# Optimization experiments

Measured on AMD Instinct MI355X. Metric: run time of the kernel, lower is better.

Reference implementation:

```python
import jax, jax.numpy as jnp
import numpy as np

H = 64  # hidden size
I = 1   # input size


def setup_inputs() -> dict:
    key = jax.random.key(0)
    ks = jax.random.split(key, 7)
    B, T = 4096, 512
    s_ih = 1.0 / np.sqrt(H)
    x = jax.random.normal(ks[0], (B, T, I), dtype=jnp.float32)
    # torch nn.GRU params: weight_ih [3H, I], weight_hh [3H, H], biases [3H]
    W_ih = jax.random.uniform(ks[1], (3 * H, I), minval=-s_ih, maxval=s_ih, dtype=jnp.float32)
    W_hh = jax.random.uniform(ks[2], (3 * H, H), minval=-s_ih, maxval=s_ih, dtype=jnp.float32)
    b_ih = jax.random.uniform(ks[3], (3 * H,), minval=-s_ih, maxval=s_ih, dtype=jnp.float32)
    b_hh = jax.random.uniform(ks[4], (3 * H,), minval=-s_ih, maxval=s_ih, dtype=jnp.float32)
    # final Linear(64, 1)
    W_out = jax.random.uniform(ks[5], (1, H), minval=-s_ih, maxval=s_ih, dtype=jnp.float32)
    b_out = jax.random.uniform(ks[6], (1,), minval=-s_ih, maxval=s_ih, dtype=jnp.float32)
    return {"x": x, "W_ih": W_ih, "W_hh": W_hh, "b_ih": b_ih, "b_hh": b_hh,
            "W_out": W_out, "b_out": b_out}


def _gru_last_hidden(x, W_ih, W_hh, b_ih, b_hh):
    B, T, _ = x.shape
    # precompute input projections for all timesteps: [B, T, 3H]
    xp = jnp.einsum('bti,gi->btg', x, W_ih) + b_ih
    xp = jnp.swapaxes(xp, 0, 1)  # [T, B, 3H]
    Whr, Whz, Whn = W_hh[:H], W_hh[H:2 * H], W_hh[2 * H:]
    bhr, bhz, bhn = b_hh[:H], b_hh[H:2 * H], b_hh[2 * H:]

    def step(h, xt):
        xr, xz, xn = xt[:, :H], xt[:, H:2 * H], xt[:, 2 * H:]
        r = jax.nn.sigmoid(xr + h @ Whr.T + bhr)
        z = jax.nn.sigmoid(xz + h @ Whz.T + bhz)
        n = jnp.tanh(xn + r * (h @ Whn.T + bhn))
        h_new = (1.0 - z) * n + z * h
        return h_new, None

    h0 = jnp.zeros((B, H), dtype=x.dtype)
    h_last, _ = jax.lax.scan(step, h0, xp)
    return h_last


def reference(x, W_ih, W_hh, b_ih, b_hh, W_out, b_out):
    h_last = _gru_last_hidden(x, W_ih, W_hh, b_ih, b_hh)
    return h_last @ W_out.T + b_out  # [B, 1]
```

## Files before the change

### kernel.cpp

```cpp
#include <hip/hip_runtime.h>
#include <stdint.h>

#define TT 512
#define BT 8
#define XSTR 516

typedef float    f32x4 __attribute__((ext_vector_type(4)));
typedef float    f32x2 __attribute__((ext_vector_type(2)));
typedef short    s16x8 __attribute__((ext_vector_type(8)));
typedef __fp16   h16x2 __attribute__((ext_vector_type(2)));
typedef _Float16 f16x8 __attribute__((ext_vector_type(8)));

#define MFMA_F16(A, B, C) \
    __builtin_amdgcn_mfma_f32_16x16x32_f16( \
        __builtin_bit_cast(f16x8, (A)), (B), (C), 0, 0, 0)

#define LOG2E  1.442695040888963f
#define LOG2E2 2.885390081777927f

__global__ __launch_bounds__(256, 2) void gru_scan_kernel(
    const float* __restrict__ x,
    const float* __restrict__ Wih,
    const float* __restrict__ Whh,
    const float* __restrict__ bih,
    const float* __restrict__ bhh,
    const float* __restrict__ Wout,
    const float* __restrict__ bout,
    float* __restrict__ out)
{
    __shared__ __align__(16) float xs[BT * XSTR];
    __shared__ __align__(16) short hbuf[2][1024];
    __shared__ float outp[4][BT];

    const int tid  = threadIdx.x;
    const int w    = tid >> 6;
    const int L    = tid & 63;
    const int n16  = L & 15;
    const int quad = L >> 4;
    const int q    = w * 16 + n16;
    const int b0   = blockIdx.x * BT;

    #pragma unroll
    for (int k = 0; k < 4; ++k) {
        int idx = tid + k * 256;
        int row = idx >> 7;
        int t4  = idx & 127;
        f32x4 v = *(const f32x4*)(x + (size_t)(b0 + row) * TT + t4 * 4);
        *(f32x4*)(xs + row * XSTR + t4 * 4) = v;
    }
    {
        f32x4* hb = (f32x4*)hbuf;
        f32x4 zv = {0.f, 0.f, 0.f, 0.f};
        hb[tid] = zv;
    }

    const float wr2   = -LOG2E  * Wih[q];
    const float wz2   = -LOG2E  * Wih[64 + q];
    const float wn2   =  LOG2E2 * Wih[128 + q];
    const float bR2   = -LOG2E  * (bih[q]      + bhh[q]);
    const float bZ2   = -LOG2E  * (bih[64 + q] + bhh[64 + q]);
    const float bN2   =  LOG2E2 * bhh[128 + q];
    const float bihn2 =  LOG2E2 * bih[128 + q];
    const float wo    = Wout[q];

    const f32x4 bR4 = {bR2, bR2, bR2, bR2};
    const f32x4 bZ4 = {bZ2, bZ2, bZ2, bZ2};
    const f32x4 bN4 = {bN2, bN2, bN2, bN2};

    f16x8 Bf[3][2];
    #pragma unroll
    for (int g = 0; g < 3; ++g) {
        const float sg = (g == 2) ? LOG2E2 : -LOG2E;
        #pragma unroll
        for (int c = 0; c < 2; ++c) {
            const float* p = Whh + ((g * 64 + q) * 64 + c * 32 + quad * 8);
            #pragma unroll
            for (int j = 0; j < 8; ++j)
                Bf[g][c][j] = (_Float16)(p[j] * sg);
        }
    }

    float hD[2] = {0.f, 0.f};

    const int kg   = q >> 3;
    const int sxor = (kg & 1) * 4;
    int waddr[2];
    #pragma unroll
    for (int p = 0; p < 2; ++p)
        waddr[p] = (kg * 16 + ((p * 4 + quad) ^ sxor)) * 8 + (q & 7);

    const int permx = ((n16 & 3) * 4 + (n16 >> 2)) ^ ((quad & 1) * 4);
    const int rslot = quad * 16 + permx;

    const s16x8* hbv = (const s16x8*)hbuf;
    const float* xrow0 = xs + (quad * 2) * XSTR;
    const float* xrow1 = xrow0 + XSTR;

    if ((blockIdx.x >> 8) & 1) __builtin_amdgcn_s_sleep(6);

    auto step = [&](int cur, f32x2 xv) {
        __syncthreads();

        s16x8 A0 = hbv[cur * 128 +  0 + rslot];
        s16x8 A1 = hbv[cur * 128 + 64 + rslot];

        f32x4 aR = MFMA_F16(A0, Bf[0][0], bR4);
        aR       = MFMA_F16(A1, Bf[0][1], aR);
        f32x4 aN = MFMA_F16(A0, Bf[2][0], bN4);
        aN       = MFMA_F16(A1, Bf[2][1], aN);
        f32x4 aZ = MFMA_F16(A0, Bf[1][0], bZ4);
        aZ       = MFMA_F16(A1, Bf[1][1], aZ);

        short* wh = (short*)hbuf + (cur ^ 1) * 1024;

        f32x2 aRp = {aR[0], aR[1]};
        f32x2 aZp = {aZ[0], aZ[1]};
        f32x2 aNp = {aN[0], aN[1]};
        f32x2 hp  = {hD[0], hD[1]};

        f32x2 ar = xv * wr2 + aRp;
        f32x2 Er = {__builtin_amdgcn_exp2f(ar[0]), __builtin_amdgcn_exp2f(ar[1])};
        f32x2 DR = Er + 1.0f;
        f32x2 r  = {__builtin_amdgcn_rcpf(DR[0]), __builtin_amdgcn_rcpf(DR[1])};
        f32x2 az = xv * wz2 + aZp;
        f32x2 Ez = {__builtin_amdgcn_exp2f(az[0]), __builtin_amdgcn_exp2f(az[1])};
        f32x2 DZ = Ez + 1.0f;
        f32x2 xn = xv * wn2 + bihn2;
        f32x2 an = r * aNp + xn;
        f32x2 En = {__builtin_amdgcn_exp2f(an[0]), __builtin_amdgcn_exp2f(an[1])};
        f32x2 DN = En + 1.0f;
        f32x2 P  = DZ * DN;
        f32x2 iq = {__builtin_amdgcn_rcpf(P[0]), __builtin_amdgcn_rcpf(P[1])};
        f32x2 z  = iq * DN;
        f32x2 rn = iq * DZ;
        f32x2 n  = rn * -2.0f + 1.0f;
        f32x2 hn = z * (hp - n) + n;

        hD[0] = hn[0]; hD[1] = hn[1];

        h16x2 hpk = __builtin_amdgcn_cvt_pkrtz(hn[0], hn[1]);
        unsigned upk = __builtin_bit_cast(unsigned, hpk);
        wh[waddr[0]] = (short)(upk & 0xffffu);
        wh[waddr[1]] = (short)(upk >> 16);
    };

    for (int t = 0; t < TT; t += 4) {
        f32x4 xa = *(const f32x4*)(xrow0 + t);
        f32x4 xb = *(const f32x4*)(xrow1 + t);
        step(0, f32x2{xa[0], xb[0]});
        step(1, f32x2{xa[1], xb[1]});
        step(0, f32x2{xa[2], xb[2]});
        step(1, f32x2{xa[3], xb[3]});
    }

    float p0 = hD[0] * wo;
    float p1 = hD[1] * wo;
    #pragma unroll
    for (int mask = 1; mask <= 8; mask <<= 1) {
        p0 += __shfl_xor(p0, mask, 64);
        p1 += __shfl_xor(p1, mask, 64);
    }
    if (n16 == 0) {
        outp[w][quad * 2]     = p0;
        outp[w][quad * 2 + 1] = p1;
    }
    __syncthreads();
    if (tid < BT) {
        out[b0 + tid] = outp[0][tid] + outp[1][tid] + outp[2][tid] + outp[3][tid] + bout[0];
    }
}

extern "C" void kernel_launch(void* const* d_in, const int* in_sizes, int n_in,
                              void* d_out, int out_size, void* d_ws, size_t ws_size,
                              hipStream_t stream) {
    (void)in_sizes; (void)n_in; (void)d_ws; (void)ws_size; (void)out_size;
    const float* x    = (const float*)d_in[0];
    const float* Wih  = (const float*)d_in[1];
    const float* Whh  = (const float*)d_in[2];
    const float* bih  = (const float*)d_in[3];
    const float* bhh  = (const float*)d_in[4];
    const float* Wout = (const float*)d_in[5];
    const float* bout = (const float*)d_in[6];
    float* out = (float*)d_out;

    gru_scan_kernel<<<dim3(4096 / BT), dim3(256), 0, stream>>>(
        x, Wih, Whh, bih, bhh, Wout, bout, out);
}
```

Measured before the change: 196.4 us.

## Process two independent 8-row batch slices per block to interleave recurrences

Each block now handles 16 batch rows as two independent 8-row GRU recurrences that share one barrier per timestep. Their MFMAs and gate math are interleaved so one chain's latency can hide behind the other's. Grid size halves and launch bounds drop to one block per SIMD group. The h update is also rewritten algebraically by carrying h-1, and the staggered sleep is removed. The trade-off is more registers and LDS per block and fewer blocks for the scheduler to overlap.

```diff
diff --git a/kernel.cpp b/kernel.cpp
--- a/kernel.cpp
+++ b/kernel.cpp
@@ -2,7 +2,7 @@
 #include <stdint.h>
 
 #define TT 512
-#define BT 8
+#define BTW 16
 #define XSTR 516
 
 typedef float    f32x4 __attribute__((ext_vector_type(4)));
@@ -18,7 +18,7 @@
 #define LOG2E  1.442695040888963f
 #define LOG2E2 2.885390081777927f
 
-__global__ __launch_bounds__(256, 2) void gru_scan_kernel(
+__global__ __launch_bounds__(256, 1) void gru_scan_kernel(
     const float* __restrict__ x,
     const float* __restrict__ Wih,
     const float* __restrict__ Whh,
@@ -28,9 +28,9 @@
     const float* __restrict__ bout,
     float* __restrict__ out)
 {
-    __shared__ __align__(16) float xs[BT * XSTR];
-    __shared__ __align__(16) short hbuf[2][1024];
-    __shared__ float outp[4][BT];
+    __shared__ __align__(16) float xs[BTW * XSTR];
+    __shared__ __align__(16) short hbuf[2][2][1024];
+    __shared__ float outp[2][4][8];
 
     const int tid  = threadIdx.x;
     const int w    = tid >> 6;
@@ -38,20 +38,20 @@
     const int n16  = L & 15;
     const int quad = L >> 4;
     const int q    = w * 16 + n16;
-    const int b0   = blockIdx.x * BT;
-
-    #pragma unroll
-    for (int k = 0; k < 4; ++k) {
+    const int bb0  = blockIdx.x * BTW;
+
+    #pragma unroll
+    for (int k = 0; k < 8; ++k) {
         int idx = tid + k * 256;
         int row = idx >> 7;
         int t4  = idx & 127;
-        f32x4 v = *(const f32x4*)(x + (size_t)(b0 + row) * TT + t4 * 4);
+        f32x4 v = *(const f32x4*)(x + (size_t)(bb0 + row) * TT + t4 * 4);
         *(f32x4*)(xs + row * XSTR + t4 * 4) = v;
     }
     {
-        f32x4* hb = (f32x4*)hbuf;
-        f32x4 zv = {0.f, 0.f, 0.f, 0.f};
-        hb[tid] = zv;
+        unsigned* hz = (unsigned*)hbuf;
+        #pragma unroll
+        for (int k = 0; k < 8; ++k) hz[tid + k * 256] = 0u;
     }
 
     const float wr2   = -LOG2E  * Wih[q];
@@ -80,8 +80,6 @@
         }
     }
 
-    float hD[2] = {0.f, 0.f};
-
     const int kg   = q >> 3;
     const int sxor = (kg & 1) * 4;
     int waddr[2];
@@ -92,51 +90,44 @@
     const int permx = ((n16 & 3) * 4 + (n16 >> 2)) ^ ((quad & 1) * 4);
     const int rslot = quad * 16 + permx;
 
-    const s16x8* hbv = (const s16x8*)hbuf;
-    const float* xrow0 = xs + (quad * 2) * XSTR;
-    const float* xrow1 = xrow0 + XSTR;
-
-    if ((blockIdx.x >> 8) & 1) __builtin_amdgcn_s_sleep(6);
-
-    auto step = [&](int cur, f32x2 xv) {
-        __syncthreads();
-
-        s16x8 A0 = hbv[cur * 128 +  0 + rslot];
-        s16x8 A1 = hbv[cur * 128 + 64 + rslot];
-
-        f32x4 aR = MFMA_F16(A0, Bf[0][0], bR4);
-        aR       = MFMA_F16(A1, Bf[0][1], aR);
-        f32x4 aN = MFMA_F16(A0, Bf[2][0], bN4);
-        aN       = MFMA_F16(A1, Bf[2][1], aN);
-        f32x4 aZ = MFMA_F16(A0, Bf[1][0], bZ4);
-        aZ       = MFMA_F16(A1, Bf[1][1], aZ);
-
-        short* wh = (short*)hbuf + (cur ^ 1) * 1024;
-
+    const s16x8* hb0 = (const s16x8*)hbuf[0];
+    const s16x8* hb1 = (const s16x8*)hbuf[1];
+
+    const float* x00 = xs + (     quad * 2    ) * XSTR;
+    const float* x01 = xs + (     quad * 2 + 1) * XSTR;
+    const float* x10 = xs + (8 +  quad * 2    ) * XSTR;
+    const float* x11 = xs + (8 +  quad * 2 + 1) * XSTR;
+
+    float hD0[2] = {0.f, 0.f};  f32x2 hm10 = {-1.f, -1.f};
+    float hD1[2] = {0.f, 0.f};  f32x2 hm11 = {-1.f, -1.f};
+
+    auto gmath = [&](const f32x4& aR, const f32x4& aN, const f32x4& aZ,
+                     f32x2 xv, f32x2& hm1v, float* hDv, short* wh) {
         f32x2 aRp = {aR[0], aR[1]};
+        f32x2 aNp = {aN[0], aN[1]};
         f32x2 aZp = {aZ[0], aZ[1]};
-        f32x2 aNp = {aN[0], aN[1]};
-        f32x2 hp  = {hD[0], hD[1]};
 
         f32x2 ar = xv * wr2 + aRp;
         f32x2 Er = {__builtin_amdgcn_exp2f(ar[0]), __builtin_amdgcn_exp2f(ar[1])};
         f32x2 DR = Er + 1.0f;
         f32x2 r  = {__builtin_amdgcn_rcpf(DR[0]), __builtin_amdgcn_rcpf(DR[1])};
-        f32x2 az = xv * wz2 + aZp;
-        f32x2 Ez = {__builtin_amdgcn_exp2f(az[0]), __builtin_amdgcn_exp2f(az[1])};
-        f32x2 DZ = Ez + 1.0f;
         f32x2 xn = xv * wn2 + bihn2;
         f32x2 an = r * aNp + xn;
         f32x2 En = {__builtin_amdgcn_exp2f(an[0]), __builtin_amdgcn_exp2f(an[1])};
         f32x2 DN = En + 1.0f;
+        f32x2 az = xv * wz2 + aZp;
+        f32x2 Ez = {__builtin_amdgcn_exp2f(az[0]), __builtin_amdgcn_exp2f(az[1])};
+        f32x2 DZ = Ez + 1.0f;
         f32x2 P  = DZ * DN;
         f32x2 iq = {__builtin_amdgcn_rcpf(P[0]), __builtin_amdgcn_rcpf(P[1])};
         f32x2 z  = iq * DN;
         f32x2 rn = iq * DZ;
         f32x2 n  = rn * -2.0f + 1.0f;
-        f32x2 hn = z * (hp - n) + n;
-
-        hD[0] = hn[0]; hD[1] = hn[1];
+        f32x2 s  = rn *  2.0f + hm1v;
+        f32x2 hn = z * s + n;
+
+        hDv[0] = hn[0]; hDv[1] = hn[1];
+        hm1v = hn - 1.0f;
 
         h16x2 hpk = __builtin_amdgcn_cvt_pkrtz(hn[0], hn[1]);
         unsigned upk = __builtin_bit_cast(unsigned, hpk);
@@ -144,29 +135,59 @@
         wh[waddr[1]] = (short)(upk >> 16);
     };
 
+    auto round = [&](int cur, f32x2 xv0, f32x2 xv1) {
+        __syncthreads();
+
+        s16x8 A00 = hb0[cur * 128 +      rslot];
+        s16x8 A01 = hb0[cur * 128 + 64 + rslot];
+        s16x8 A10 = hb1[cur * 128 +      rslot];
+        s16x8 A11 = hb1[cur * 128 + 64 + rslot];
+
+        f32x4 aR0 = MFMA_F16(A00, Bf[0][0], bR4); aR0 = MFMA_F16(A01, Bf[0][1], aR0);
+        f32x4 aN0 = MFMA_F16(A00, Bf[2][0], bN4); aN0 = MFMA_F16(A01, Bf[2][1], aN0);
+        f32x4 aZ0 = MFMA_F16(A00, Bf[1][0], bZ4); aZ0 = MFMA_F16(A01, Bf[1][1], aZ0);
+        f32x4 aR1 = MFMA_F16(A10, Bf[0][0], bR4); aR1 = MFMA_F16(A11, Bf[0][1], aR1);
+        f32x4 aN1 = MFMA_F16(A10, Bf[2][0], bN4); aN1 = MFMA_F16(A11, Bf[2][1], aN1);
+        f32x4 aZ1 = MFMA_F16(A10, Bf[1][0], bZ4); aZ1 = MFMA_F16(A11, Bf[1][1], aZ1);
+
+        gmath(aR0, aN0, aZ0, xv0, hm10, hD0, (short*)hbuf[0] + (cur ^ 1) * 1024);
+        gmath(aR1, aN1, aZ1, xv1, hm11, hD1, (short*)hbuf[1] + (cur ^ 1) * 1024);
+    };
+
     for (int t = 0; t < TT; t += 4) {
-        f32x4 xa = *(const f32x4*)(xrow0 + t);
-        f32x4 xb = *(const f32x4*)(xrow1 + t);
-        step(0, f32x2{xa[0], xb[0]});
-        step(1, f32x2{xa[1], xb[1]});
-        step(0, f32x2{xa[2], xb[2]});
-        step(1, f32x2{xa[3], xb[3]});
-    }
-
-    float p0 = hD[0] * wo;
-    float p1 = hD[1] * wo;
+        f32x4 xa0 = *(const f32x4*)(x00 + t);
+        f32x4 xb0 = *(const f32x4*)(x01 + t);
+        f32x4 xa1 = *(const f32x4*)(x10 + t);
+        f32x4 xb1 = *(const f32x4*)(x11 + t);
+        round(0, f32x2{xa0[0], xb0[0]}, f32x2{xa1[0], xb1[0]});
+        round(1, f32x2{xa0[1], xb0[1]}, f32x2{xa1[1], xb1[1]});
+        round(0, f32x2{xa0[2], xb0[2]}, f32x2{xa1[2], xb1[2]});
+        round(1, f32x2{xa0[3], xb0[3]}, f32x2{xa1[3], xb1[3]});
+    }
+
+    float p00 = hD0[0] * wo;
+    float p01 = hD0[1] * wo;
+    float p10 = hD1[0] * wo;
+    float p11 = hD1[1] * wo;
     #pragma unroll
     for (int mask = 1; mask <= 8; mask <<= 1) {
-        p0 += __shfl_xor(p0, mask, 64);
-        p1 += __shfl_xor(p1, mask, 64);
+        p00 += __shfl_xor(p00, mask, 64);
+        p01 += __shfl_xor(p01, mask, 64);
+        p10 += __shfl_xor(p10, mask, 64);
+        p11 += __shfl_xor(p11, mask, 64);
     }
     if (n16 == 0) {
-        outp[w][quad * 2]     = p0;
-        outp[w][quad * 2 + 1] = p1;
+        outp[0][w][quad * 2]     = p00;
+        outp[0][w][quad * 2 + 1] = p01;
+        outp[1][w][quad * 2]     = p10;
+        outp[1][w][quad * 2 + 1] = p11;
     }
     __syncthreads();
-    if (tid < BT) {
-        out[b0 + tid] = outp[0][tid] + outp[1][tid] + outp[2][tid] + outp[3][tid] + bout[0];
+    if (tid < BTW) {
+        int ss = tid >> 3;
+        int c  = tid & 7;
+        out[bb0 + tid] = outp[ss][0][c] + outp[ss][1][c] +
+                         outp[ss][2][c] + outp[ss][3][c] + bout[0];
     }
 }
 
@@ -183,6 +204,6 @@
     const float* bout = (const float*)d_in[6];
     float* out = (float*)d_out;
 
-    gru_scan_kernel<<<dim3(4096 / BT), dim3(256), 0, stream>>>(
+    gru_scan_kernel<<<dim3(4096 / BTW), dim3(256), 0, stream>>>(
         x, Wih, Whh, bih, bhh, Wout, bout, out);
 }
```

Result: slower. 249.6 us (+27.1%).

## Merge two batch tiles per block with spin-wait sub-barriers and pacing

Applied to the files above, without the earlier changes.

Each block now holds two independent 8-row batch sets of four waves each, launched as 512 threads. Per-step __syncthreads is replaced by a spin barrier on LDS counters scoped to each set. Set 1 is paced to run about one step behind set 0 through a shared 'pace' flag, so the two sets' MFMA and transcendental phases interleave instead of contending. This removes block-wide barriers and the old s_sleep staggering between blocks. It risks spin-loop overhead and relies on volatile LDS polling being correctly ordered.

```diff
diff --git a/kernel.cpp b/kernel.cpp
--- a/kernel.cpp
+++ b/kernel.cpp
@@ -2,7 +2,6 @@
 #include <stdint.h>
 
 #define TT 512
-#define BT 8
 #define XSTR 516
 
 typedef float    f32x4 __attribute__((ext_vector_type(4)));
@@ -18,7 +17,7 @@
 #define LOG2E  1.442695040888963f
 #define LOG2E2 2.885390081777927f
 
-__global__ __launch_bounds__(256, 2) void gru_scan_kernel(
+__global__ __launch_bounds__(512, 1) void gru_scan_kernel(
     const float* __restrict__ x,
     const float* __restrict__ Wih,
     const float* __restrict__ Whh,
@@ -28,31 +27,37 @@
     const float* __restrict__ bout,
     float* __restrict__ out)
 {
-    __shared__ __align__(16) float xs[BT * XSTR];
-    __shared__ __align__(16) short hbuf[2][1024];
-    __shared__ float outp[4][BT];
+    __shared__ __align__(16) float xs[16 * XSTR];
+    __shared__ __align__(16) short hbuf[2][2][1024];
+    __shared__ int   cnt[2][4];
+    __shared__ int   pace;
+    __shared__ float outp[8][8];
 
     const int tid  = threadIdx.x;
     const int w    = tid >> 6;
+    const int set  = w >> 2;
+    const int wv   = w & 3;
     const int L    = tid & 63;
     const int n16  = L & 15;
     const int quad = L >> 4;
-    const int q    = w * 16 + n16;
-    const int b0   = blockIdx.x * BT;
+    const int q    = wv * 16 + n16;
+    const int bb0  = blockIdx.x * 16;
 
     #pragma unroll
     for (int k = 0; k < 4; ++k) {
-        int idx = tid + k * 256;
+        int idx = tid + k * 512;
         int row = idx >> 7;
         int t4  = idx & 127;
-        f32x4 v = *(const f32x4*)(x + (size_t)(b0 + row) * TT + t4 * 4);
+        f32x4 v = *(const f32x4*)(x + (size_t)(bb0 + row) * TT + t4 * 4);
         *(f32x4*)(xs + row * XSTR + t4 * 4) = v;
     }
     {
-        f32x4* hb = (f32x4*)hbuf;
-        f32x4 zv = {0.f, 0.f, 0.f, 0.f};
-        hb[tid] = zv;
-    }
+        unsigned* hz = (unsigned*)hbuf;
+        #pragma unroll
+        for (int k = 0; k < 4; ++k) hz[tid + k * 512] = 0u;
+    }
+    if (tid < 8) ((int*)cnt)[tid] = 0;
+    if (tid == 8) pace = 0;
 
     const float wr2   = -LOG2E  * Wih[q];
     const float wz2   = -LOG2E  * Wih[64 + q];
@@ -92,66 +97,81 @@
     const int permx = ((n16 & 3) * 4 + (n16 >> 2)) ^ ((quad & 1) * 4);
     const int rslot = quad * 16 + permx;
 
-    const s16x8* hbv = (const s16x8*)hbuf;
-    const float* xrow0 = xs + (quad * 2) * XSTR;
+    const s16x8* hbv = (const s16x8*)hbuf[set];
+    const float* xrow0 = xs + (set * 8 + quad * 2) * XSTR;
     const float* xrow1 = xrow0 + XSTR;
 
-    if ((blockIdx.x >> 8) & 1) __builtin_amdgcn_s_sleep(6);
-
-    auto step = [&](int cur, f32x2 xv) {
-        __syncthreads();
-
-        s16x8 A0 = hbv[cur * 128 +  0 + rslot];
-        s16x8 A1 = hbv[cur * 128 + 64 + rslot];
-
-        f32x4 aR = MFMA_F16(A0, Bf[0][0], bR4);
-        aR       = MFMA_F16(A1, Bf[0][1], aR);
-        f32x4 aN = MFMA_F16(A0, Bf[2][0], bN4);
-        aN       = MFMA_F16(A1, Bf[2][1], aN);
-        f32x4 aZ = MFMA_F16(A0, Bf[1][0], bZ4);
-        aZ       = MFMA_F16(A1, Bf[1][1], aZ);
-
-        short* wh = (short*)hbuf + (cur ^ 1) * 1024;
-
-        f32x2 aRp = {aR[0], aR[1]};
-        f32x2 aZp = {aZ[0], aZ[1]};
-        f32x2 aNp = {aN[0], aN[1]};
-        f32x2 hp  = {hD[0], hD[1]};
-
-        f32x2 ar = xv * wr2 + aRp;
-        f32x2 Er = {__builtin_amdgcn_exp2f(ar[0]), __builtin_amdgcn_exp2f(ar[1])};
-        f32x2 DR = Er + 1.0f;
-        f32x2 r  = {__builtin_amdgcn_rcpf(DR[0]), __builtin_amdgcn_rcpf(DR[1])};
-        f32x2 az = xv * wz2 + aZp;
-        f32x2 Ez = {__builtin_amdgcn_exp2f(az[0]), __builtin_amdgcn_exp2f(az[1])};
-        f32x2 DZ = Ez + 1.0f;
-        f32x2 xn = xv * wn2 + bihn2;
-        f32x2 an = r * aNp + xn;
-        f32x2 En = {__builtin_amdgcn_exp2f(an[0]), __builtin_amdgcn_exp2f(an[1])};
-        f32x2 DN = En + 1.0f;
-        f32x2 P  = DZ * DN;
-        f32x2 iq = {__builtin_amdgcn_rcpf(P[0]), __builtin_amdgcn_rcpf(P[1])};
-        f32x2 z  = iq * DN;
-        f32x2 rn = iq * DZ;
-        f32x2 n  = rn * -2.0f + 1.0f;
-        f32x2 hn = z * (hp - n) + n;
-
-        hD[0] = hn[0]; hD[1] = hn[1];
-
-        h16x2 hpk = __builtin_amdgcn_cvt_pkrtz(hn[0], hn[1]);
-        unsigned upk = __builtin_bit_cast(unsigned, hpk);
-        wh[waddr[0]] = (short)(upk & 0xffffu);
-        wh[waddr[1]] = (short)(upk >> 16);
+    __syncthreads();
+
+    auto sbar = [&](int v) {
+        __threadfence_block();
+        if (L == 0) ((volatile int*)cnt[set])[wv] = v;
+        volatile int* c = (volatile int*)cnt[set];
+        while (c[0] < v || c[1] < v || c[2] < v || c[3] < v) { }
+        __threadfence_block();
     };
 
+    int s = 0;
     for (int t = 0; t < TT; t += 4) {
         f32x4 xa = *(const f32x4*)(xrow0 + t);
         f32x4 xb = *(const f32x4*)(xrow1 + t);
-        step(0, f32x2{xa[0], xb[0]});
-        step(1, f32x2{xa[1], xb[1]});
-        step(0, f32x2{xa[2], xb[2]});
-        step(1, f32x2{xa[3], xb[3]});
-    }
+        #pragma unroll
+        for (int j = 0; j < 4; ++j) {
+            f32x2 xv = {xa[j], xb[j]};
+            ++s;
+
+            if (set) {
+                volatile int* pp = &pace;
+                while (*pp < s + 1) __builtin_amdgcn_s_sleep(1);
+            }
+            sbar(s);
+
+            const int cur = (s - 1) & 1;
+            s16x8 A0 = hbv[cur * 128 +  0 + rslot];
+            s16x8 A1 = hbv[cur * 128 + 64 + rslot];
+
+            f32x4 aR = MFMA_F16(A0, Bf[0][0], bR4);
+            aR       = MFMA_F16(A1, Bf[0][1], aR);
+            f32x4 aN = MFMA_F16(A0, Bf[2][0], bN4);
+            aN       = MFMA_F16(A1, Bf[2][1], aN);
+            f32x4 aZ = MFMA_F16(A0, Bf[1][0], bZ4);
+            aZ       = MFMA_F16(A1, Bf[1][1], aZ);
+
+            if (!set && w == 0 && L == 0) *(volatile int*)&pace = s;
+
+            f32x2 aRp = {aR[0], aR[1]};
+            f32x2 aZp = {aZ[0], aZ[1]};
+            f32x2 aNp = {aN[0], aN[1]};
+            f32x2 hp  = {hD[0], hD[1]};
+
+            f32x2 ar = xv * wr2 + aRp;
+            f32x2 Er = {__builtin_amdgcn_exp2f(ar[0]), __builtin_amdgcn_exp2f(ar[1])};
+            f32x2 DR = Er + 1.0f;
+            f32x2 r  = {__builtin_amdgcn_rcpf(DR[0]), __builtin_amdgcn_rcpf(DR[1])};
+            f32x2 az = xv * wz2 + aZp;
+            f32x2 Ez = {__builtin_amdgcn_exp2f(az[0]), __builtin_amdgcn_exp2f(az[1])};
+            f32x2 DZ = Ez + 1.0f;
+            f32x2 xn = xv * wn2 + bihn2;
+            f32x2 an = r * aNp + xn;
+            f32x2 En = {__builtin_amdgcn_exp2f(an[0]), __builtin_amdgcn_exp2f(an[1])};
+            f32x2 DN = En + 1.0f;
+            f32x2 P  = DZ * DN;
+            f32x2 iq = {__builtin_amdgcn_rcpf(P[0]), __builtin_amdgcn_rcpf(P[1])};
+            f32x2 z  = iq * DN;
+            f32x2 rn = iq * DZ;
+            f32x2 n  = rn * -2.0f + 1.0f;
+            f32x2 hn = z * (hp - n) + n;
+
+            hD[0] = hn[0]; hD[1] = hn[1];
+
+            h16x2 hpk = __builtin_amdgcn_cvt_pkrtz(hn[0], hn[1]);
+            unsigned upk = __builtin_bit_cast(unsigned, hpk);
+            short* wh = (short*)hbuf[set] + (cur ^ 1) * 1024;
+            wh[waddr[0]] = (short)(upk & 0xffffu);
+            wh[waddr[1]] = (short)(upk >> 16);
+        }
+    }
+    if (!set && w == 0 && L == 0) *(volatile int*)&pace = TT + 1;
 
     float p0 = hD[0] * wo;
     float p1 = hD[1] * wo;
@@ -165,8 +185,11 @@
         outp[w][quad * 2 + 1] = p1;
     }
     __syncthreads();
-    if (tid < BT) {
-        out[b0 + tid] = outp[0][tid] + outp[1][tid] + outp[2][tid] + outp[3][tid] + bout[0];
+    if (tid < 16) {
+        int ss = tid >> 3;
+        int c  = tid & 7;
+        out[bb0 + tid] = outp[ss * 4 + 0][c] + outp[ss * 4 + 1][c] +
+                         outp[ss * 4 + 2][c] + outp[ss * 4 + 3][c] + bout[0];
     }
 }
 
@@ -183,6 +206,6 @@
     const float* bout = (const float*)d_in[6];
     float* out = (float*)d_out;
 
-    gru_scan_kernel<<<dim3(4096 / BT), dim3(256), 0, stream>>>(
+    gru_scan_kernel<<<dim3(4096 / 16), dim3(512), 0, stream>>>(
         x, Wih, Whh, bih, bhh, Wout, bout, out);
 }
```

Result: slower. 327.1 us (+66.5%).
